# Optimization experiments

Hardware: AMD Instinct MI355X
Metric: run time of the kernel (lower is better)

Reference implementation:

```python
import jax, jax.numpy as jnp
import numpy as np
from jax import lax

B, C, L, G = 2048, 9605, 20, 50
ALPHA, ALPHA1, ALPHA2, ALPHA3, ALPHA_OTHER = 0.5, 0.05, 2.0, 10.0, 0.5
NEG_INF = jnp.float32(-1e30)


def setup_inputs() -> dict:
    k0, k1, k2, k3 = jax.random.split(jax.random.key(0), 4)
    x = jax.random.normal(k0, (B, C), jnp.float32)
    # sparse multi-label targets (~10 positives/row) so at most ~1 whitelist group is active,
    # matching the original code's assert len(gt_whitelist_index) == 1
    y = (jax.random.uniform(k1, (B, C)) < 0.001).astype(jnp.int32)
    y_neg = (jax.random.uniform(k2, (B, C)) < 0.001).astype(jnp.int32)
    # L disjoint whitelist groups of G classes each (from mapping_dict in the original)
    idx = jax.random.permutation(k3, C)[: L * G].reshape(L, G)
    group_mask = jnp.zeros((L, C), bool).at[jnp.arange(L)[:, None], idx].set(True)
    return {"x": x, "y": y, "y_neg": y_neg, "group_mask": group_mask}


def _rank_loss(x1, x2, margin):
    # our_rank_loss: sigmoid(alpha3*(x2-x1+margin)), scaled by alpha2 when positive
    d = x2 - x1 + margin
    s = jax.nn.sigmoid(ALPHA3 * d)
    return jnp.where(d > 0, ALPHA2 * s, s)


def reference(x, y, y_neg, group_mask):
    xs = jax.nn.sigmoid(x)  # [B, C]
    gmf = group_mask.astype(jnp.float32)  # [L, C]

    # per-row max score inside each whitelist group -> [B, L]
    # lax.map over the L (=20) groups keeps peak memory at one [B, C] temp per step
    group_max = lax.map(
        lambda m: jnp.max(jnp.where(m, xs, NEG_INF), axis=-1), group_mask
    ).T  # [B, L]

    # find_gt_whitelist: group k active iff sum(y[group_k]) > 0
    active = jnp.einsum("bc,lc->bl", y.astype(jnp.float32), gmf) > 0
    active_neg = jnp.einsum("bc,lc->bl", y_neg.astype(jnp.float32), gmf) > 0
    has_gt = jnp.any(active, axis=-1)  # [B]
    g = jnp.argmax(active, axis=-1)  # first active group (original asserts exactly one)

    # top_k_thres = max(11th largest sigmoid score, alpha_other) in both branches
    thres = jnp.maximum(lax.top_k(xs, 11)[0][:, 10], ALPHA_OTHER)  # [B]

    # max over union of all whitelist classes (wl_indices)
    union_max = jnp.max(jnp.where(jnp.any(group_mask, 0)[None, :], xs, NEG_INF), -1)

    gt_max = jnp.take_along_axis(group_max, g[:, None], axis=1)[:, 0]  # [B]
    # incorrect_max: max(0, max over groups != g); incorrect_neg: max(0, max over neg-active groups)
    excl = jnp.where(jnp.arange(L)[None, :] == g[:, None], NEG_INF, group_max)
    incorrect_max = jnp.maximum(jnp.max(excl, -1), 0.0)
    incorrect_neg = jnp.maximum(jnp.max(jnp.where(active_neg, group_max, 0.0), -1), 0.0)

    # branch A: no gt whitelist group active
    case_a = (1 - ALPHA) * _rank_loss(thres, union_max, ALPHA1) + ALPHA * _rank_loss(
        thres, incorrect_neg, ALPHA1
    )
    # branch B: exactly one gt group g
    case_b = (
        _rank_loss(gt_max, thres, ALPHA1)
        + jnp.where(
            incorrect_max > 0, (1 - ALPHA) * _rank_loss(thres, incorrect_max, ALPHA1), 0.0
        )
        + jnp.where(
            incorrect_neg > 0,
            ALPHA * _rank_loss(thres, incorrect_neg, ALPHA1),
            ALPHA * _rank_loss(thres, incorrect_max, ALPHA1),
        )
    )
    return jnp.sum(jnp.where(has_gt, case_b, case_a))
```

## Files before the change

kernel.cpp:

```cpp
#include <hip/hip_runtime.h>
#include <stdint.h>

#define B_ROWS 2048
#define C_CLS  9605
#define L_GRP  20
#define GM_BYTES (L_GRP * C_CLS)
#define REPSTRIDE 9728
#define GID_REGION (4 * REPSTRIDE)
#define PCOUNT_OFF (64 + GID_REGION)
#define NEG_BIG -3.0e38f

typedef float f32x4 __attribute__((ext_vector_type(4)));
typedef unsigned u32x4 __attribute__((ext_vector_type(4)));

__device__ __forceinline__ float sigmoidf(float v) {
  return 1.0f / (1.0f + __expf(-v));
}

__device__ __forceinline__ float rank_loss(float x1, float x2) {
  float d = x2 - x1 + 0.05f;
  float s = 1.0f / (1.0f + __expf(-10.0f * d));
  return d > 0.0f ? 2.0f * s : s;
}

__device__ __forceinline__ unsigned fmap(float f) {
  unsigned u = __float_as_uint(f);
  return (u & 0x80000000u) ? ~u : (u | 0x80000000u);
}
__device__ __forceinline__ float funmap(unsigned m) {
  unsigned u = (m & 0x80000000u) ? (m ^ 0x80000000u) : ~m;
  return __uint_as_float(u);
}

__global__ __launch_bounds__(256) void probe_init_kernel(
    const uint4* __restrict__ gm, unsigned char* __restrict__ ws,
    float* __restrict__ out, int* __restrict__ pcount) {
  __shared__ int s_part[4];
  const int tid = threadIdx.x;
  const int bid = blockIdx.x;
  const int gtid = bid * 256 + tid;

  if (gtid == 0) out[0] = 0.0f;
  uint4* gfill = (uint4*)(ws + 64);
  const unsigned F = 0xFFFFFFFFu;
  if (gtid < GID_REGION / 16) gfill[gtid] = make_uint4(F, F, F, F);

  int local = 0;
  const int nvec = GM_BYTES / 16;
  if (gtid < nvec) {
    uint4 w = gm[gtid];
    unsigned a[4] = {w.x, w.y, w.z, w.w};
#pragma unroll
    for (int q = 0; q < 4; ++q) {
      local += ((a[q] & 0x000000FFu) != 0) + ((a[q] & 0x0000FF00u) != 0) +
               ((a[q] & 0x00FF0000u) != 0) + ((a[q] & 0xFF000000u) != 0);
    }
  } else if (gtid == nvec) {
    unsigned a = ((const unsigned*)gm)[nvec * 4];
    local += ((a & 0x000000FFu) != 0) + ((a & 0x0000FF00u) != 0) +
             ((a & 0x00FF0000u) != 0) + ((a & 0xFF000000u) != 0);
  }
#pragma unroll
  for (int off = 32; off; off >>= 1) local += __shfl_xor(local, off);
  if ((tid & 63) == 0) s_part[tid >> 6] = local;
  __syncthreads();
  if (tid == 0) pcount[bid] = s_part[0] + s_part[1] + s_part[2] + s_part[3];
}

__global__ __launch_bounds__(256) void build_gid_kernel(
    const void* gm, const int* __restrict__ pcount,
    unsigned char* __restrict__ ws) {
  __shared__ int s_part[4];
  __shared__ int s_total;
  const int tid = threadIdx.x;
  int v = pcount[tid];
#pragma unroll
  for (int off = 32; off; off >>= 1) v += __shfl_xor(v, off);
  if ((tid & 63) == 0) s_part[tid >> 6] = v;
  __syncthreads();
  if (tid == 0) s_total = s_part[0] + s_part[1] + s_part[2] + s_part[3];
  __syncthreads();
  const bool is_byte = (s_total > 600);

  const int i = blockIdx.x * 256 + tid;
  if (i >= GM_BYTES) return;
  bool m;
  if (is_byte) m = ((const unsigned char*)gm)[i] != 0;
  else         m = ((const unsigned int*)gm)[i] != 0u;
  if (m) {
    int l = i / C_CLS;
    int c = i - l * C_CLS;
    unsigned char* base = ws + 64;
#pragma unroll
    for (int r = 0; r < 4; ++r) base[r * REPSTRIDE + r + c] = (unsigned char)l;
  }
}

__global__ __launch_bounds__(256, 8) void loss_kernel(
    const float* __restrict__ x, const int* __restrict__ y,
    const int* __restrict__ yn, const unsigned char* __restrict__ ws64,
    float* __restrict__ out) {
  __shared__ unsigned s_gmax[L_GRP];
  __shared__ unsigned s_act, s_actn;
  __shared__ float s_wtop[4 * 11];
  const int tid = threadIdx.x;
  const int lane = tid & 63;
  const int wave = tid >> 6;
  const int row = blockIdx.x;

  const size_t base = (size_t)row * C_CLS;
  const int mis = (int)(base & 3);
  const int peel = (4 - mis) & 3;
  const float* xr = x + base;
  const int* yr = y + base;
  const int* nr = yn + base;
  const unsigned char* gidc = ws64 + mis * REPSTRIDE + mis;

  if (tid < L_GRP) s_gmax[tid] = 0u;
  if (tid == 0) { s_act = 0u; s_actn = 0u; }
  __syncthreads();

  float t[11];
#pragma unroll
  for (int i = 0; i < 11; ++i) t[i] = 0.0f;
  unsigned actL = 0u, actnL = 0u;

  auto ins = [&](float v) {
    if (v > t[10]) {
      float a = v;
#pragma unroll
      for (int i = 0; i < 11; ++i) {
        float hi = fmaxf(t[i], a); a = fminf(t[i], a); t[i] = hi;
      }
    }
  };
  auto gmax_upd = [&](unsigned gk, float v) {
    unsigned fm = fmap(v);
    if (fm > s_gmax[gk]) atomicMax(&s_gmax[gk], fm);
  };
  auto edge = [&](int c) {
    float v = xr[c];
    ins(v);
    unsigned gk = gidc[c];
    if (gk < L_GRP) {
      gmax_upd(gk, v);
      unsigned bit = 1u << gk;
      if (yr[c] != 0) actL |= bit;
      if (nr[c] != 0) actnL |= bit;
    }
  };

  if (tid < peel) edge(tid);
  const int nvec = (C_CLS - peel) >> 2;
  const int tail0 = peel + (nvec << 2);
  if (tid < C_CLS - tail0) edge(tail0 + tid);

  const f32x4* x4 = (const f32x4*)(xr + peel);
  const u32x4* y4 = (const u32x4*)(yr + peel);
  const u32x4* n4 = (const u32x4*)(nr + peel);
  const unsigned* g4 = (const unsigned*)(gidc + peel);

  for (int j = tid; j < nvec; j += 256) {
    f32x4 xv = __builtin_nontemporal_load(x4 + j);
    u32x4 yv = __builtin_nontemporal_load(y4 + j);
    u32x4 nv = __builtin_nontemporal_load(n4 + j);
    unsigned gw = g4[j];

    if (gw != 0xFFFFFFFFu) {
      unsigned g0 = gw & 0xFFu, g1 = (gw >> 8) & 0xFFu,
               g2 = (gw >> 16) & 0xFFu, g3 = gw >> 24;
      if (g0 < L_GRP) gmax_upd(g0, xv.x);
      if (g1 < L_GRP) gmax_upd(g1, xv.y);
      if (g2 < L_GRP) gmax_upd(g2, xv.z);
      if (g3 < L_GRP) gmax_upd(g3, xv.w);
    }
    if (yv.x | yv.y | yv.z | yv.w | nv.x | nv.y | nv.z | nv.w) {
      const unsigned yq[4] = {yv.x, yv.y, yv.z, yv.w};
      const unsigned nq[4] = {nv.x, nv.y, nv.z, nv.w};
      const unsigned gq[4] = {gw & 0xFFu, (gw >> 8) & 0xFFu,
                              (gw >> 16) & 0xFFu, gw >> 24};
#pragma unroll
      for (int q = 0; q < 4; ++q) {
        if ((yq[q] | nq[q]) && gq[q] < L_GRP) {
          unsigned bit = 1u << gq[q];
          if (yq[q]) actL |= bit;
          if (nq[q]) actnL |= bit;
        }
      }
    }
    float am = fmaxf(fmaxf(xv.x, xv.y), fmaxf(xv.z, xv.w));
    if (am > t[10]) { ins(xv.x); ins(xv.y); ins(xv.z); ins(xv.w); }
  }

  if (actL) atomicOr(&s_act, actL);
  if (actnL) atomicOr(&s_actn, actnL);

  float cur = t[0];
  float mr[11];
#pragma unroll
  for (int r = 0; r < 11; ++r) {
    float m = cur;
#pragma unroll
    for (int off = 32; off; off >>= 1) m = fmaxf(m, __shfl_xor(m, off));
    mr[r] = m;
    if (r < 10) {
      unsigned long long b = __ballot(cur == m);
      int leader = (int)(__ffsll(b) - 1);
      if (lane == leader) {
#pragma unroll
        for (int i = 0; i < 10; ++i) t[i] = t[i + 1];
        t[10] = NEG_BIG;
        cur = t[0];
      }
    }
  }
  if (lane == 0) {
#pragma unroll
    for (int r = 0; r < 11; ++r) s_wtop[wave * 11 + r] = mr[r];
  }
  __syncthreads();

  if (wave == 0) {
    float v = (lane < 44) ? s_wtop[lane] : NEG_BIG;
    float eleventh = NEG_BIG;
#pragma unroll
    for (int r = 0; r < 11; ++r) {
      float m = v;
#pragma unroll
      for (int off = 32; off; off >>= 1) m = fmaxf(m, __shfl_xor(m, off));
      eleventh = m;
      if (r < 10) {
        unsigned long long b = __ballot(v == m);
        int leader = (int)(__ffsll(b) - 1);
        if (lane == leader) v = NEG_BIG;
      }
    }

    const unsigned aL = s_act, anL = s_actn;
    const bool has_gt = (aL != 0u);
    const int g = has_gt ? (__ffs(aL) - 1) : 0;
    const float thres = fmaxf(sigmoidf(eleventh), 0.5f);

    float union_max = NEG_BIG, gt_sg = 0.0f, inc_max = NEG_BIG, inc_neg = 0.0f;
#pragma unroll
    for (int l = 0; l < L_GRP; ++l) {
      float sg = sigmoidf(funmap(s_gmax[l]));
      union_max = fmaxf(union_max, sg);
      if (l == g) gt_sg = sg; else inc_max = fmaxf(inc_max, sg);
      if ((anL >> l) & 1u) inc_neg = fmaxf(inc_neg, sg);
    }
    inc_max = fmaxf(inc_max, 0.0f);
    inc_neg = fmaxf(inc_neg, 0.0f);

    float loss;
    if (has_gt) {
      loss = rank_loss(gt_sg, thres);
      if (inc_max > 0.0f) loss += 0.5f * rank_loss(thres, inc_max);
      loss += 0.5f * rank_loss(thres, (inc_neg > 0.0f) ? inc_neg : inc_max);
    } else {
      loss = 0.5f * rank_loss(thres, union_max) + 0.5f * rank_loss(thres, inc_neg);
    }
    if (lane == 0) atomicAdd(out, loss);
  }
}

extern "C" void kernel_launch(void* const* d_in, const int* in_sizes, int n_in,
                              void* d_out, int out_size, void* d_ws, size_t ws_size,
                              hipStream_t stream) {
  (void)in_sizes; (void)n_in; (void)out_size; (void)ws_size;
  const float* x = (const float*)d_in[0];
  const int* y = (const int*)d_in[1];
  const int* yn = (const int*)d_in[2];
  const void* gm = d_in[3];

  unsigned char* ws = (unsigned char*)d_ws;
  unsigned char* ws64 = ws + 64;
  int* pcount = (int*)(ws + PCOUNT_OFF);

  probe_init_kernel<<<256, 256, 0, stream>>>((const uint4*)gm, ws,
                                             (float*)d_out, pcount);
  build_gid_kernel<<<(GM_BYTES + 255) / 256, 256, 0, stream>>>(gm, pcount, ws);
  loss_kernel<<<B_ROWS, 256, 0, stream>>>(x, y, yn, ws64, (float*)d_out);
}
```

Measured before the change: 237.0 us.

## Merge mask probe into gid build and use fmed3 top-k insertion

The separate probe/init kernel is folded into the gid-building kernel. Each of its 38 blocks now redundantly scans the whole group mask to detect the dtype, and each thread writes the group id for one class column by looping over the 20 groups. This drops one launch and the 0xFF fill pass. The top-11 insertion in the loss kernel now uses a chain of fmed3 operations instead of paired fmax/fmin, which cuts the instruction count per insert. The cost is redundant mask reads in every block of the setup kernel.

```diff
diff --git a/kernel.cpp b/kernel.cpp
--- a/kernel.cpp
+++ b/kernel.cpp
@@ -7,7 +7,6 @@
 #define GM_BYTES (L_GRP * C_CLS)
 #define REPSTRIDE 9728
 #define GID_REGION (4 * REPSTRIDE)
-#define PCOUNT_OFF (64 + GID_REGION)
 #define NEG_BIG -3.0e38f
 
 typedef float f32x4 __attribute__((ext_vector_type(4)));
@@ -32,30 +31,28 @@
   return __uint_as_float(u);
 }
 
-__global__ __launch_bounds__(256) void probe_init_kernel(
-    const uint4* __restrict__ gm, unsigned char* __restrict__ ws,
-    float* __restrict__ out, int* __restrict__ pcount) {
+__global__ __launch_bounds__(256) void build_gid_kernel(
+    const void* __restrict__ gm, unsigned char* __restrict__ ws,
+    float* __restrict__ out) {
   __shared__ int s_part[4];
+  __shared__ int s_total;
   const int tid = threadIdx.x;
-  const int bid = blockIdx.x;
-  const int gtid = bid * 256 + tid;
-
-  if (gtid == 0) out[0] = 0.0f;
-  uint4* gfill = (uint4*)(ws + 64);
-  const unsigned F = 0xFFFFFFFFu;
-  if (gtid < GID_REGION / 16) gfill[gtid] = make_uint4(F, F, F, F);
+  const int c = blockIdx.x * 256 + tid;
+  if (c == 0) out[0] = 0.0f;
 
   int local = 0;
+  const uint4* gm16 = (const uint4*)gm;
   const int nvec = GM_BYTES / 16;
-  if (gtid < nvec) {
-    uint4 w = gm[gtid];
+  for (int i = tid; i < nvec; i += 256) {
+    uint4 w = gm16[i];
     unsigned a[4] = {w.x, w.y, w.z, w.w};
 #pragma unroll
     for (int q = 0; q < 4; ++q) {
       local += ((a[q] & 0x000000FFu) != 0) + ((a[q] & 0x0000FF00u) != 0) +
                ((a[q] & 0x00FF0000u) != 0) + ((a[q] & 0xFF000000u) != 0);
     }
-  } else if (gtid == nvec) {
+  }
+  if (tid == 0) {
     unsigned a = ((const unsigned*)gm)[nvec * 4];
     local += ((a & 0x000000FFu) != 0) + ((a & 0x0000FF00u) != 0) +
              ((a & 0x00FF0000u) != 0) + ((a & 0xFF000000u) != 0);
@@ -64,36 +61,26 @@
   for (int off = 32; off; off >>= 1) local += __shfl_xor(local, off);
   if ((tid & 63) == 0) s_part[tid >> 6] = local;
   __syncthreads();
-  if (tid == 0) pcount[bid] = s_part[0] + s_part[1] + s_part[2] + s_part[3];
-}
-
-__global__ __launch_bounds__(256) void build_gid_kernel(
-    const void* gm, const int* __restrict__ pcount,
-    unsigned char* __restrict__ ws) {
-  __shared__ int s_part[4];
-  __shared__ int s_total;
-  const int tid = threadIdx.x;
-  int v = pcount[tid];
-#pragma unroll
-  for (int off = 32; off; off >>= 1) v += __shfl_xor(v, off);
-  if ((tid & 63) == 0) s_part[tid >> 6] = v;
-  __syncthreads();
   if (tid == 0) s_total = s_part[0] + s_part[1] + s_part[2] + s_part[3];
   __syncthreads();
   const bool is_byte = (s_total > 600);
 
-  const int i = blockIdx.x * 256 + tid;
-  if (i >= GM_BYTES) return;
-  bool m;
-  if (is_byte) m = ((const unsigned char*)gm)[i] != 0;
-  else         m = ((const unsigned int*)gm)[i] != 0u;
-  if (m) {
-    int l = i / C_CLS;
-    int c = i - l * C_CLS;
-    unsigned char* base = ws + 64;
-#pragma unroll
-    for (int r = 0; r < 4; ++r) base[r * REPSTRIDE + r + c] = (unsigned char)l;
-  }
+  if (c >= C_CLS) return;
+  unsigned char g = 0xFF;
+  if (is_byte) {
+    const unsigned char* m8 = (const unsigned char*)gm;
+#pragma unroll
+    for (int l = L_GRP - 1; l >= 0; --l)
+      if (m8[l * C_CLS + c] != 0) g = (unsigned char)l;
+  } else {
+    const unsigned* m32 = (const unsigned*)gm;
+#pragma unroll
+    for (int l = L_GRP - 1; l >= 0; --l)
+      if (m32[l * C_CLS + c] != 0u) g = (unsigned char)l;
+  }
+  unsigned char* base = ws + 64;
+#pragma unroll
+  for (int r = 0; r < 4; ++r) base[r * REPSTRIDE + r + c] = g;
 }
 
 __global__ __launch_bounds__(256, 8) void loss_kernel(
@@ -127,11 +114,10 @@
 
   auto ins = [&](float v) {
     if (v > t[10]) {
-      float a = v;
-#pragma unroll
-      for (int i = 0; i < 11; ++i) {
-        float hi = fmaxf(t[i], a); a = fminf(t[i], a); t[i] = hi;
-      }
+#pragma unroll
+      for (int i = 10; i >= 1; --i)
+        t[i] = __builtin_amdgcn_fmed3f(v, t[i - 1], t[i]);
+      t[0] = fmaxf(t[0], v);
     }
   };
   auto gmax_upd = [&](unsigned gk, float v) {
@@ -275,10 +261,8 @@
 
   unsigned char* ws = (unsigned char*)d_ws;
   unsigned char* ws64 = ws + 64;
-  int* pcount = (int*)(ws + PCOUNT_OFF);
-
-  probe_init_kernel<<<256, 256, 0, stream>>>((const uint4*)gm, ws,
-                                             (float*)d_out, pcount);
-  build_gid_kernel<<<(GM_BYTES + 255) / 256, 256, 0, stream>>>(gm, pcount, ws);
+
+  build_gid_kernel<<<(C_CLS + 255) / 256, 256, 0, stream>>>(gm, ws,
+                                                            (float*)d_out);
   loss_kernel<<<B_ROWS, 256, 0, stream>>>(x, y, yn, ws64, (float*)d_out);
 }
```

Result: slower. 245.7 us (+3.7%).
